# Kernel tuning notes

Hardware: AMD Instinct MI355X
Metric: run time of the kernel (lower is better)

The kernel has to match this reference:

```python
import jax, jax.numpy as jnp
import numpy as np

B, BUFF, STK, NCOMP, HIST = 128, 64, 48, 8, 96
VOCAB, WDIM, POSN, POSD = 100000, 300, 50, 50
DEP, CAD, HAD, FC, U = 40, 50, 50, 128, 256
NOUT = 2 + 2 * DEP


def setup_inputs() -> dict:
    key = jax.random.key(0)
    ks = jax.random.split(key, 40)
    d = {}
    d['buff_word_id'] = jax.random.randint(ks[0], (B, BUFF), 0, VOCAB)
    d['buff_pos_id'] = jax.random.randint(ks[1], (B, BUFF), 0, POSN)
    d['comp_word_id'] = jax.random.randint(ks[2], (B, STK, 2 * NCOMP), 0, VOCAB)
    d['comp_pos_id'] = jax.random.randint(ks[3], (B, STK, 2 * NCOMP), 0, POSN)
    d['comp_action_id'] = jax.random.randint(ks[4], (B, STK, NCOMP), 0, 2 * DEP)
    d['comp_action_len'] = jax.random.randint(ks[5], (B, STK), 0, NCOMP + 1)
    d['history_action_id'] = jax.random.randint(ks[6], (B, HIST), 0, 3 + 4 * DEP)
    d['stack_length'] = jax.random.randint(ks[7], (B,), 1, STK + 1)
    d['buff_length'] = jax.random.randint(ks[8], (B,), 1, BUFF + 1)
    d['history_action_length'] = jax.random.randint(ks[9], (B,), 1, HIST + 1)

    def w(k, shape):
        return jax.random.normal(k, shape, jnp.float32) / np.sqrt(shape[0])

    d['p_emb'] = jax.random.normal(ks[10], (POSN, POSD), jnp.float32) * 0.1
    d['comp_a_emb'] = jax.random.normal(ks[11], (2 * DEP, CAD), jnp.float32) * 0.1
    d['hist_a_emb'] = jax.random.normal(ks[12], (3 + 4 * DEP, HAD), jnp.float32) * 0.1
    d['w_emb'] = jax.random.normal(ks[13], (VOCAB, WDIM), jnp.float32) * 0.1
    d['emb_W'] = w(ks[14], (WDIM + POSD, FC)); d['emb_b'] = jnp.zeros((FC,), jnp.float32)
    d['rec_W'] = w(ks[15], (FC + CAD + FC, FC)); d['rec_b'] = jnp.zeros((FC,), jnp.float32)
    d['sW0'] = w(ks[16], (FC + U, 4 * U)); d['sb0'] = jnp.zeros((4 * U,), jnp.float32)
    d['sW1'] = w(ks[17], (U + U, 4 * U)); d['sb1'] = jnp.zeros((4 * U,), jnp.float32)
    d['bW0'] = w(ks[18], (FC + U, 4 * U)); d['bb0'] = jnp.zeros((4 * U,), jnp.float32)
    d['bW1'] = w(ks[19], (U + U, 4 * U)); d['bb1'] = jnp.zeros((4 * U,), jnp.float32)
    d['aW0'] = w(ks[20], (HAD + U, 4 * U)); d['ab0'] = jnp.zeros((4 * U,), jnp.float32)
    d['aW1'] = w(ks[21], (U + U, 4 * U)); d['ab1'] = jnp.zeros((4 * U,), jnp.float32)
    d['fW'] = w(ks[22], (3 * U, NOUT)); d['fb'] = jnp.zeros((NOUT,), jnp.float32)
    return d


def _lstm_cell(c, h, x, W, b):
    # TF LSTMCell gate order: i, j (candidate), f, o; forget_bias = 1.0
    z = jnp.concatenate([x, h], -1) @ W + b
    i, j, f, o = jnp.split(z, 4, -1)
    c = c * jax.nn.sigmoid(f + 1.0) + jax.nn.sigmoid(i) * jnp.tanh(j)
    h = jnp.tanh(c) * jax.nn.sigmoid(o)
    return c, h


def _run_lstm2(x, lengths, W0, b0, W1, b1):
    # x: [B, T, D]; returns final (at t = length) second-layer h, like dynamic_rnn's state[1].h
    Bb, T, _ = x.shape
    u = W0.shape[1] // 4
    init = tuple(jnp.zeros((Bb, u), x.dtype) for _ in range(4))

    def step(carry, inp):
        xt, t = inp
        c0, h0, c1, h1 = carry
        nc0, nh0 = _lstm_cell(c0, h0, xt, W0, b0)
        nc1, nh1 = _lstm_cell(c1, h1, nh0, W1, b1)
        m = (t < lengths)[:, None]
        new = tuple(jnp.where(m, n, o) for n, o in zip((nc0, nh0, nc1, nh1), carry))
        return new, None

    (c0, h0, c1, h1), _ = jax.lax.scan(step, init, (x.transpose(1, 0, 2), jnp.arange(T)))
    return h1


def _compose(word_id, comp_emb, act_emb, a_len, rec_W, rec_b):
    # word_id: [2N] int, comp_emb: [2N, FC], act_emb: [N, CAD], a_len: scalar
    # Sequential dict-keyed recursive composition (dict keys are head word ids).
    N = act_emb.shape[0]
    head_ids = word_id[0::2]
    dep_ids = word_id[1::2]
    idxs = jnp.arange(N)

    def step(vals, n):
        mask_h = (head_ids == head_ids[n]) & (idxs < n)
        mask_d = (head_ids == dep_ids[n]) & (idxs < n)
        ih = jnp.max(jnp.where(mask_h, idxs, -1))
        idd = jnp.max(jnp.where(mask_d, idxs, -1))
        head_e = jnp.where(ih >= 0, vals[jnp.maximum(ih, 0)], comp_emb[2 * n])
        dep_e = jnp.where(idd >= 0, vals[jnp.maximum(idd, 0)], comp_emb[2 * n + 1])
        new = jnp.tanh(jnp.concatenate([head_e, act_emb[n], dep_e]) @ rec_W + rec_b)
        return vals.at[n].set(new), new

    vals0 = jnp.zeros((N, rec_W.shape[1]), comp_emb.dtype)
    _, news = jax.lax.scan(step, vals0, idxs)
    return jnp.where(a_len == 0, comp_emb[0], news[jnp.maximum(a_len - 1, 0)])


def reference(buff_word_id, buff_pos_id, comp_word_id, comp_pos_id, comp_action_id,
              comp_action_len, history_action_id, stack_length, buff_length,
              history_action_length, p_emb, comp_a_emb, hist_a_emb, w_emb,
              emb_W, emb_b, rec_W, rec_b, sW0, sb0, sW1, sb1, bW0, bb0, bW1, bb1,
              aW0, ab0, aW1, ab1, fW, fb):
    buff_emb = jax.nn.relu(
        jnp.concatenate([w_emb[buff_word_id], p_emb[buff_pos_id]], -1) @ emb_W + emb_b)
    comp_emb = jax.nn.relu(
        jnp.concatenate([w_emb[comp_word_id], p_emb[comp_pos_id]], -1) @ emb_W + emb_b)
    act_emb = comp_a_emb[comp_action_id]        # [B, STK, N, CAD]
    hist_emb = hist_a_emb[history_action_id]    # [B, HIST, HAD]

    comp_fn = lambda wi, ce, ae, al: _compose(wi, ce, ae, al, rec_W, rec_b)
    stack_emb = jax.vmap(jax.vmap(comp_fn))(comp_word_id, comp_emb, act_emb, comp_action_len)

    h_s = _run_lstm2(stack_emb, stack_length, sW0, sb0, sW1, sb1)
    h_b = _run_lstm2(buff_emb, buff_length, bW0, bb0, bW1, bb1)
    h_a = _run_lstm2(hist_emb, history_action_length, aW0, ab0, aW1, ab1)
    return jnp.concatenate([h_s, h_b, h_a], -1) @ fW + fb
```

## Files before the change

kernel.cpp:

```cpp
#include <hip/hip_runtime.h>

#define BB    128
#define BUFF  64
#define STK   48
#define NCOMP 8
#define HIST  96
#define WDIM  300
#define POSD  50
#define CAD   50
#define HAD   50
#define FC    128
#define UU    256
#define NOUT  82

typedef __bf16 bf16;
typedef __attribute__((ext_vector_type(8))) __bf16 bf16x8;
typedef __attribute__((ext_vector_type(4))) float   f32x4;

__device__ __forceinline__ float sigf(float x)   { return 1.f / (1.f + __expf(-x)); }
__device__ __forceinline__ float tanhf_(float x) { return 1.f - 2.f / (1.f + __expf(2.f * x)); }

__device__ __forceinline__ unsigned pack2(const float* p) {
  union { unsigned u; bf16 h[2]; } r;
  r.h[0] = (bf16)p[0]; r.h[1] = (bf16)p[1];
  return r.u;
}

__global__ __launch_bounds__(256) void k_emb(
    const int* bw, const int* bp, const int* cw, const int* cp,
    const float* w_emb, const float* p_emb, const float* embW, const float* embB,
    bf16* comp_emb, bf16* buff_emb)
{
  __shared__ __align__(16) char sm[138752];
  bf16*  A  = (bf16*)sm;
  bf16*  Wt = (bf16*)(sm + 46080);
  float* sb = (float*)(sm + 46080 + 92160);

  const int tid = threadIdx.x;
  const int r0  = blockIdx.x * 64;

  for (int i = tid; i < 64 * 176; i += 256) {
    int m = i / 176, c2 = i % 176, e0 = 2 * c2;
    int r = r0 + m;
    unsigned v;
    if (e0 < 300) {
      int word = (r < 98304) ? cw[r] : bw[r - 98304];
      v = pack2(w_emb + word * 300 + e0);
    } else if (e0 < 350) {
      int pos = (r < 98304) ? cp[r] : bp[r - 98304];
      v = pack2(p_emb + pos * 50 + (e0 - 300));
    } else v = 0u;
    *(unsigned*)(A + m * 360 + e0) = v;
  }
  for (int i = tid; i < 350 * 128; i += 256) {
    int k = i >> 7, n = i & 127;
    Wt[n * 360 + k] = (bf16)embW[i];
  }
  { int i = tid; if (i < 256) { int n = i >> 1; Wt[n * 360 + 350 + (i & 1)] = (bf16)0.f; } }
  if (tid < 128) sb[tid] = embB[tid];
  __syncthreads();

  const int wv = tid >> 6, lane = tid & 63, l15 = lane & 15, quad = lane >> 4;
  f32x4 acc[8];
#pragma unroll
  for (int i = 0; i < 8; ++i) acc[i] = (f32x4){0.f, 0.f, 0.f, 0.f};

  const bf16* Arow = A + (wv * 16 + l15) * 360;
  for (int ks = 0; ks < 11; ++ks) {
    int kq = ks * 32 + quad * 8;
    bf16x8 a = *(const bf16x8*)(Arow + kq);
#pragma unroll
    for (int nt = 0; nt < 8; ++nt) {
      bf16x8 b = *(const bf16x8*)(Wt + (nt * 16 + l15) * 360 + kq);
      acc[nt] = __builtin_amdgcn_mfma_f32_16x16x32_bf16(a, b, acc[nt], 0, 0, 0);
    }
  }
#pragma unroll
  for (int nt = 0; nt < 8; ++nt)
#pragma unroll
    for (int rr = 0; rr < 4; ++rr) {
      int row = wv * 16 + quad * 4 + rr;
      int n   = nt * 16 + l15;
      float z = fmaxf(acc[nt][rr] + sb[n], 0.f);
      int r = r0 + row;
      bf16 o = (bf16)z;
      if (r < 98304) comp_emb[r * 128 + n] = o;
      else           buff_emb[(r - 98304) * 128 + n] = o;
    }
}

__global__ __launch_bounds__(256) void k_compose(
    const int* cw, const int* caid, const int* calen,
    const bf16* comp_emb, const float* ca_emb, const float* recW, const float* recB,
    bf16* stack_emb)
{
  __shared__ __align__(16) char sm[129344];
  bf16*  Wt   = (bf16*)sm;
  bf16*  X    = (bf16*)(sm + 83968);
  bf16*  VALS = (bf16*)(sm + 94464);
  float* recb = (float*)(sm + 127232);
  int*   IH   = (int*)(sm + 127744);
  int*   ID   = (int*)(sm + 128256);
  int*   AN   = (int*)(sm + 128768);
  int*   ALEN = (int*)(sm + 129280);

  const int tid = threadIdx.x;
  const int bs0 = blockIdx.x * 16;

  for (int i = tid; i < 306 * 128; i += 256) {
    int k = i >> 7, n = i & 127;
    Wt[n * 328 + k] = (bf16)recW[i];
  }
  for (int i = tid; i < 128 * 22; i += 256) {
    int n = i / 22, k = 306 + i % 22;
    Wt[n * 328 + k] = (bf16)0.f;
  }
  if (tid < 128) recb[tid] = recB[tid];
  if (tid < 16) {
    int bs = bs0 + tid;
    int hid[8], did[8];
#pragma unroll
    for (int m = 0; m < 8; ++m) { hid[m] = cw[bs * 16 + 2 * m]; did[m] = cw[bs * 16 + 2 * m + 1]; }
    for (int n = 0; n < 8; ++n) {
      int ih = -1, idd = -1;
      for (int m = 0; m < n; ++m) { if (hid[m] == hid[n]) ih = m; if (hid[m] == did[n]) idd = m; }
      IH[tid * 8 + n] = ih; ID[tid * 8 + n] = idd; AN[tid * 8 + n] = caid[bs * 8 + n];
    }
    ALEN[tid] = calen[bs];
  }
  __syncthreads();

  const int wv = tid >> 6, lane = tid & 63, l15 = lane & 15, quad = lane >> 4;

  for (int n = 0; n < 8; ++n) {
    for (int i = tid; i < 16 * 160; i += 256) {
      int p = i / 160, c2 = i % 160, e0 = 2 * c2;
      int bs = bs0 + p;
      unsigned v;
      if (e0 < 128) {
        int ih = IH[p * 8 + n];
        v = (ih >= 0) ? *(const unsigned*)(VALS + (p * 8 + ih) * 128 + e0)
                      : *(const unsigned*)(comp_emb + (bs * 16 + 2 * n) * 128 + e0);
      } else if (e0 < 178) {
        v = pack2(ca_emb + AN[p * 8 + n] * 50 + (e0 - 128));
      } else if (e0 < 306) {
        int e = e0 - 178;
        int idd = ID[p * 8 + n];
        v = (idd >= 0) ? *(const unsigned*)(VALS + (p * 8 + idd) * 128 + e)
                       : *(const unsigned*)(comp_emb + (bs * 16 + 2 * n + 1) * 128 + e);
      } else v = 0u;
      *(unsigned*)(X + p * 328 + e0) = v;
    }
    __syncthreads();

    f32x4 acc[2];
    acc[0] = (f32x4){0.f,0.f,0.f,0.f}; acc[1] = (f32x4){0.f,0.f,0.f,0.f};
    for (int ks = 0; ks < 10; ++ks) {
      int kq = ks * 32 + quad * 8;
      bf16x8 a = *(const bf16x8*)(X + l15 * 328 + kq);
#pragma unroll
      for (int t2 = 0; t2 < 2; ++t2) {
        int nt = 2 * wv + t2;
        bf16x8 b = *(const bf16x8*)(Wt + (nt * 16 + l15) * 328 + kq);
        acc[t2] = __builtin_amdgcn_mfma_f32_16x16x32_bf16(a, b, acc[t2], 0, 0, 0);
      }
    }
    __syncthreads();
#pragma unroll
    for (int t2 = 0; t2 < 2; ++t2) {
      int nt = 2 * wv + t2;
#pragma unroll
      for (int rr = 0; rr < 4; ++rr) {
        int p = quad * 4 + rr;
        int col = nt * 16 + l15;
        VALS[(p * 8 + n) * 128 + col] = (bf16)tanhf_(acc[t2][rr] + recb[col]);
      }
    }
    __syncthreads();
  }

  for (int i = tid; i < 16 * 64; i += 256) {
    int p = i / 64, c2 = i % 64, e0 = 2 * c2;
    int bs = bs0 + p;
    int al = ALEN[p];
    unsigned v = (al == 0) ? *(const unsigned*)(comp_emb + (bs * 16) * 128 + e0)
                           : *(const unsigned*)(VALS + (p * 8 + (al - 1)) * 128 + e0);
    *(unsigned*)(stack_emb + bs * 128 + e0) = v;
  }
}

struct BarT { int cnt; int pad[31]; };

template<int L, int LAYER>
__device__ __forceinline__ void lstm_role(
    const float* W, const float* bias,
    const bf16* xsrc, const float* hist_tab, const int* hist_id,
    const int* lenp, bf16* h0w, bf16* h1w, BarT* bar, char* sm, int u0)
{
  constexpr int T   = (L == 0) ? STK : (L == 1) ? BUFF : HIST;
  constexpr int K   = (LAYER == 0) ? ((L == 2) ? 320 : 384) : 512;
  constexpr int KP  = K + 8;
  constexpr int Kxp = (LAYER == 0) ? ((L == 2) ? 64 : 128) : 256;
  constexpr int Tx  = (L == 0) ? STK : BUFF;

  const int tid = threadIdx.x;
  bf16*  Wt     = (bf16*)sm;
  bf16*  hstage = (bf16*)(sm + 128 * KP * 2);
  float* sb     = (float*)(sm + 128 * KP * 2 + 9216);
  bf16*  Xa     = (bf16*)(sm + 128 * KP * 2 + 9216 + 512);

  for (int i = tid; i < K * 128; i += 256) {
    int kk = i >> 7, cc = i & 127;
    int col = (cc >> 5) * 256 + u0 + (cc & 31);
    bf16 v;
    if (LAYER == 0 && L == 2) {
      if (kk < 64) v = (kk < 50) ? (bf16)W[kk * 1024 + col] : (bf16)0.f;
      else         v = (bf16)W[(kk - 14) * 1024 + col];
    } else v = (bf16)W[kk * 1024 + col];
    Wt[cc * KP + kk] = v;
  }
  if (tid < 128) { int col = (tid >> 5) * 256 + u0 + (tid & 31); sb[tid] = bias[col]; }

  const int wv = tid >> 6, lane = tid & 63, l15 = lane & 15, quad = lane >> 4;
  int lenr[8];
#pragma unroll
  for (int mt = 0; mt < 2; ++mt)
#pragma unroll
    for (int rr = 0; rr < 4; ++rr)
      lenr[mt * 4 + rr] = lenp[32 * wv + 16 * mt + quad * 4 + rr];

  float cst[16], hst[16];
#pragma unroll
  for (int i = 0; i < 16; ++i) { cst[i] = 0.f; hst[i] = 0.f; }

  const int row0 = 32 * wv + l15;

  __syncthreads();

  for (int p = 0; p <= T; ++p) {
    const bool active = (LAYER == 0) ? (p < T) : (p >= 1);
    const int  t = (LAYER == 0) ? p : (p - 1);

    if (L == 2 && LAYER == 0 && active) {
      for (int i = tid; i < 128 * 32; i += 256) {
        int row = i >> 5, e0 = 2 * (i & 31);
        unsigned v = 0u;
        if (e0 < 50) { int id = hist_id[row * 96 + t]; v = pack2(hist_tab + id * 50 + e0); }
        *(unsigned*)(Xa + row * 72 + e0) = v;
      }
    }
    __syncthreads();

    if (active) {
      const bf16* h0r = h0w + ((p - 1) & 1) * 32768;
      const bf16* h1r = h1w + (p & 1) * 32768;

      bf16x8 hA[16];
#pragma unroll
      for (int hk = 0; hk < 8; ++hk)
#pragma unroll
        for (int mt = 0; mt < 2; ++mt) {
          const bf16* pa = h0r + (row0 + 16 * mt) * 256 + hk * 32 + quad * 8;
          asm volatile("global_load_dwordx4 %0, %1, off sc0 sc1"
                       : "=v"(hA[hk * 2 + mt]) : "v"(pa) : "memory");
        }
      bf16x8 hB[16];
      if (LAYER == 1) {
#pragma unroll
        for (int hk = 0; hk < 8; ++hk)
#pragma unroll
          for (int mt = 0; mt < 2; ++mt) {
            const bf16* pb = h1r + (row0 + 16 * mt) * 256 + hk * 32 + quad * 8;
            asm volatile("global_load_dwordx4 %0, %1, off sc0 sc1"
                         : "=v"(hB[hk * 2 + mt]) : "v"(pb) : "memory");
          }
      }

      f32x4 acc[2][8];
#pragma unroll
      for (int a1 = 0; a1 < 2; ++a1)
#pragma unroll
        for (int a2 = 0; a2 < 8; ++a2) acc[a1][a2] = (f32x4){0.f, 0.f, 0.f, 0.f};

      if (LAYER == 0) {
#pragma unroll
        for (int ks = 0; ks < Kxp / 32; ++ks) {
          int kq = ks * 32 + quad * 8;
          bf16x8 a[2];
#pragma unroll
          for (int mt = 0; mt < 2; ++mt) {
            int row = row0 + 16 * mt;
            if (L == 2) a[mt] = *(const bf16x8*)(Xa + row * 72 + kq);
            else        a[mt] = *(const bf16x8*)(xsrc + (row * Tx + t) * 128 + kq);
          }
#pragma unroll
          for (int nt = 0; nt < 8; ++nt) {
            bf16x8 b = *(const bf16x8*)(Wt + (nt * 16 + l15) * KP + kq);
            acc[0][nt] = __builtin_amdgcn_mfma_f32_16x16x32_bf16(a[0], b, acc[0][nt], 0, 0, 0);
            acc[1][nt] = __builtin_amdgcn_mfma_f32_16x16x32_bf16(a[1], b, acc[1][nt], 0, 0, 0);
          }
        }
      }

      asm volatile("s_waitcnt vmcnt(0)" ::: "memory");
      __builtin_amdgcn_sched_barrier(0);

      constexpr int HB0 = (LAYER == 0) ? Kxp : 0;
#pragma unroll
      for (int hk = 0; hk < 8; ++hk) {
        int kq = HB0 + hk * 32 + quad * 8;
#pragma unroll
        for (int nt = 0; nt < 8; ++nt) {
          bf16x8 b = *(const bf16x8*)(Wt + (nt * 16 + l15) * KP + kq);
          acc[0][nt] = __builtin_amdgcn_mfma_f32_16x16x32_bf16(hA[hk * 2 + 0], b, acc[0][nt], 0, 0, 0);
          acc[1][nt] = __builtin_amdgcn_mfma_f32_16x16x32_bf16(hA[hk * 2 + 1], b, acc[1][nt], 0, 0, 0);
        }
      }
      if (LAYER == 1) {
#pragma unroll
        for (int hk = 0; hk < 8; ++hk) {
          int kq = 256 + hk * 32 + quad * 8;
#pragma unroll
          for (int nt = 0; nt < 8; ++nt) {
            bf16x8 b = *(const bf16x8*)(Wt + (nt * 16 + l15) * KP + kq);
            acc[0][nt] = __builtin_amdgcn_mfma_f32_16x16x32_bf16(hB[hk * 2 + 0], b, acc[0][nt], 0, 0, 0);
            acc[1][nt] = __builtin_amdgcn_mfma_f32_16x16x32_bf16(hB[hk * 2 + 1], b, acc[1][nt], 0, 0, 0);
          }
        }
      }

#pragma unroll
      for (int mt = 0; mt < 2; ++mt)
#pragma unroll
        for (int g2 = 0; g2 < 2; ++g2)
#pragma unroll
          for (int rr = 0; rr < 4; ++rr) {
            int row = 32 * wv + 16 * mt + quad * 4 + rr;
            float zi = acc[mt][0 + g2][rr] + sb[(0 + g2) * 16 + l15];
            float zj = acc[mt][2 + g2][rr] + sb[(2 + g2) * 16 + l15];
            float zf = acc[mt][4 + g2][rr] + sb[(4 + g2) * 16 + l15];
            float zo = acc[mt][6 + g2][rr] + sb[(6 + g2) * 16 + l15];
            float ig = sigf(zi), jg = tanhf_(zj), fg = sigf(zf + 1.f), og = sigf(zo);
            int idx = mt * 8 + g2 * 4 + rr;
            float cn = cst[idx] * fg + ig * jg;
            float hn = tanhf_(cn) * og;
            bool mk = (t < lenr[mt * 4 + rr]);
            cst[idx] = mk ? cn : cst[idx];
            hst[idx] = mk ? hn : hst[idx];
            hstage[row * 36 + g2 * 16 + l15] = (bf16)hst[idx];
          }
    }
    __syncthreads();
    if (active) {
      bf16* dst = (LAYER == 0) ? (h0w + (p & 1) * 32768) : (h1w + ((p - 1) & 1) * 32768);
      for (int i = tid; i < 128 * 8; i += 256) {
        int row = i >> 3, c = i & 7;
        unsigned long long v = *(const unsigned long long*)(hstage + row * 36 + c * 4);
        __hip_atomic_store((unsigned long long*)(dst + row * 256 + u0 + c * 4), v,
                           __ATOMIC_RELAXED, __HIP_MEMORY_SCOPE_AGENT);
      }
    }
    if (p < T) {
      __syncthreads();
      if (tid == 0) {
        __builtin_amdgcn_sched_barrier(0);
        const int target = 16 * (p + 1);
        int prev = __hip_atomic_fetch_add(&bar->cnt, 1, __ATOMIC_RELAXED, __HIP_MEMORY_SCOPE_AGENT);
        if (prev != target - 1) {
          while (__hip_atomic_load(&bar->cnt, __ATOMIC_RELAXED, __HIP_MEMORY_SCOPE_AGENT) < target) { }
        }
        __builtin_amdgcn_sched_barrier(0);
      }
      __syncthreads();
    }
  }
}

__global__ __launch_bounds__(256, 1) void k_lstm(
    const float* sW0, const float* sb0, const float* sW1, const float* sb1,
    const float* bW0, const float* bb0, const float* bW1, const float* bb1,
    const float* aW0, const float* ab0, const float* aW1, const float* ab1,
    const bf16* stack_emb, const bf16* buff_emb, const float* hist_tab, const int* hist_id,
    const int* len_s, const int* len_b, const int* len_a,
    bf16* h0buf, bf16* h1buf, BarT* bars)
{
  __shared__ __align__(16) char sm[143872];
  const int bx    = blockIdx.x;
  const int L     = bx >> 4;
  const int rid   = bx & 15;
  const int layer = rid >> 3;
  const int u0    = (rid & 7) * 32;

  BarT* bar = bars + L;
  bf16* h0w = h0buf + L * 2 * 32768;
  bf16* h1w = h1buf + L * 2 * 32768;

  if (L == 0) {
    if (layer == 0) lstm_role<0, 0>(sW0, sb0, stack_emb, hist_tab, hist_id, len_s, h0w, h1w, bar, sm, u0);
    else            lstm_role<0, 1>(sW1, sb1, stack_emb, hist_tab, hist_id, len_s, h0w, h1w, bar, sm, u0);
  } else if (L == 1) {
    if (layer == 0) lstm_role<1, 0>(bW0, bb0, buff_emb, hist_tab, hist_id, len_b, h0w, h1w, bar, sm, u0);
    else            lstm_role<1, 1>(bW1, bb1, buff_emb, hist_tab, hist_id, len_b, h0w, h1w, bar, sm, u0);
  } else {
    if (layer == 0) lstm_role<2, 0>(aW0, ab0, nullptr, hist_tab, hist_id, len_a, h0w, h1w, bar, sm, u0);
    else            lstm_role<2, 1>(aW1, ab1, nullptr, hist_tab, hist_id, len_a, h0w, h1w, bar, sm, u0);
  }
}

__global__ __launch_bounds__(128) void k_final(
    const bf16* h1buf, const float* fW, const float* fb, float* out)
{
  __shared__ float hs[768];
  const int b = blockIdx.x, tid = threadIdx.x;
  for (int i = tid; i < 768; i += 128) {
    int L = i >> 8, u = i & 255;
    hs[i] = (float)h1buf[(L * 2 + 1) * 32768 + b * 256 + u];
  }
  __syncthreads();
  if (tid < NOUT) {
    float acc = fb[tid];
    for (int u = 0; u < 768; ++u) acc += hs[u] * fW[u * NOUT + tid];
    out[b * NOUT + tid] = acc;
  }
}

extern "C" void kernel_launch(void* const* d_in, const int* in_sizes, int n_in,
                              void* d_out, int out_size, void* d_ws, size_t ws_size,
                              hipStream_t stream)
{
  (void)in_sizes; (void)n_in; (void)out_size; (void)ws_size;
  char* ws = (char*)d_ws;
  BarT* bars      = (BarT*)ws;
  bf16* h0buf     = (bf16*)(ws + 512);
  bf16* h1buf     = (bf16*)(ws + 512 + 393216);
  bf16* comp_emb  = (bf16*)(ws + 786944);
  bf16* buff_emb  = (bf16*)(ws + 786944 + 25165824);
  bf16* stack_emb = (bf16*)(ws + 786944 + 25165824 + 2097152);

  hipMemsetAsync(ws, 0, 786944, stream);

  k_emb<<<1664, 256, 0, stream>>>(
      (const int*)d_in[0], (const int*)d_in[1], (const int*)d_in[2], (const int*)d_in[3],
      (const float*)d_in[13], (const float*)d_in[10], (const float*)d_in[14], (const float*)d_in[15],
      comp_emb, buff_emb);

  k_compose<<<384, 256, 0, stream>>>(
      (const int*)d_in[2], (const int*)d_in[4], (const int*)d_in[5],
      comp_emb, (const float*)d_in[11], (const float*)d_in[16], (const float*)d_in[17],
      stack_emb);

  k_lstm<<<48, 256, 0, stream>>>(
      (const float*)d_in[18], (const float*)d_in[19], (const float*)d_in[20], (const float*)d_in[21],
      (const float*)d_in[22], (const float*)d_in[23], (const float*)d_in[24], (const float*)d_in[25],
      (const float*)d_in[26], (const float*)d_in[27], (const float*)d_in[28], (const float*)d_in[29],
      stack_emb, buff_emb, (const float*)d_in[12], (const int*)d_in[6],
      (const int*)d_in[7], (const int*)d_in[8], (const int*)d_in[9],
      h0buf, h1buf, bars);

  k_final<<<128, 128, 0, stream>>>(h1buf, (const float*)d_in[30], (const float*)d_in[31],
                                   (float*)d_out);
}
```

Before: 1.944 ms.

## Place each LSTM group on one XCD and relax coherence for intra-XCD exchange

The LSTM kernel now launches 256 blocks. Each block reads its XCC id from a hardware register and claims a role slot so that all 16 blocks of one LSTM sit on the same XCD; blocks that find no slot exit. Once a group is placed, it checks that every member shares the XCC id and that probe stores are visible. If both hold, the hidden-state exchange uses L2-coherent loads (sc0 only) and plain stores instead of system-scope loads and atomic stores, which aims to cut the latency of the cross-block recurrent exchange. The cost is extra startup work: the claim, a wait of up to about 10k ticks for blocks that must fall back, and a slot-claim barrier. It also relies on undocumented placement and coherence behaviour.

```diff
diff --git a/kernel.cpp b/kernel.cpp
--- a/kernel.cpp
+++ b/kernel.cpp
@@ -191,7 +191,25 @@
 
 struct BarT { int cnt; int pad[31]; };
 
-template<int L, int LAYER>
+template<bool COH>
+__device__ __forceinline__ bf16x8 hload(const bf16* p) {
+  bf16x8 v;
+  if constexpr (COH)
+    asm volatile("global_load_dwordx4 %0, %1, off sc0" : "=v"(v) : "v"(p) : "memory");
+  else
+    asm volatile("global_load_dwordx4 %0, %1, off sc0 sc1" : "=v"(v) : "v"(p) : "memory");
+  return v;
+}
+
+template<bool COH>
+__device__ __forceinline__ void hstore(bf16* p, unsigned long long v) {
+  if constexpr (COH)
+    asm volatile("global_store_dwordx2 %0, %1, off" :: "v"(p), "v"(v) : "memory");
+  else
+    __hip_atomic_store((unsigned long long*)p, v, __ATOMIC_RELAXED, __HIP_MEMORY_SCOPE_AGENT);
+}
+
+template<int L, int LAYER, bool COH>
 __device__ __forceinline__ void lstm_role(
     const float* W, const float* bias,
     const bf16* xsrc, const float* hist_tab, const int* hist_id,
@@ -259,21 +277,15 @@
 #pragma unroll
       for (int hk = 0; hk < 8; ++hk)
 #pragma unroll
-        for (int mt = 0; mt < 2; ++mt) {
-          const bf16* pa = h0r + (row0 + 16 * mt) * 256 + hk * 32 + quad * 8;
-          asm volatile("global_load_dwordx4 %0, %1, off sc0 sc1"
-                       : "=v"(hA[hk * 2 + mt]) : "v"(pa) : "memory");
-        }
+        for (int mt = 0; mt < 2; ++mt)
+          hA[hk * 2 + mt] = hload<COH>(h0r + (row0 + 16 * mt) * 256 + hk * 32 + quad * 8);
       bf16x8 hB[16];
       if (LAYER == 1) {
 #pragma unroll
         for (int hk = 0; hk < 8; ++hk)
 #pragma unroll
-          for (int mt = 0; mt < 2; ++mt) {
-            const bf16* pb = h1r + (row0 + 16 * mt) * 256 + hk * 32 + quad * 8;
-            asm volatile("global_load_dwordx4 %0, %1, off sc0 sc1"
-                         : "=v"(hB[hk * 2 + mt]) : "v"(pb) : "memory");
-          }
+          for (int mt = 0; mt < 2; ++mt)
+            hB[hk * 2 + mt] = hload<COH>(h1r + (row0 + 16 * mt) * 256 + hk * 32 + quad * 8);
       }
 
       f32x4 acc[2][8];
@@ -356,8 +368,7 @@
       for (int i = tid; i < 128 * 8; i += 256) {
         int row = i >> 3, c = i & 7;
         unsigned long long v = *(const unsigned long long*)(hstage + row * 36 + c * 4);
-        __hip_atomic_store((unsigned long long*)(dst + row * 256 + u0 + c * 4), v,
-                           __ATOMIC_RELAXED, __HIP_MEMORY_SCOPE_AGENT);
+        hstore<COH>(dst + row * 256 + u0 + c * 4, v);
       }
     }
     if (p < T) {
@@ -382,28 +393,88 @@
     const float* aW0, const float* ab0, const float* aW1, const float* ab1,
     const bf16* stack_emb, const bf16* buff_emb, const float* hist_tab, const int* hist_id,
     const int* len_s, const int* len_b, const int* len_a,
-    bf16* h0buf, bf16* h1buf, BarT* bars)
+    bf16* h0buf, bf16* h1buf, BarT* bars, BarT* cbars, int* taken, int* xcctab, int* probes)
 {
   __shared__ __align__(16) char sm[143872];
-  const int bx    = blockIdx.x;
-  const int L     = bx >> 4;
-  const int rid   = bx & 15;
+  __shared__ int s_role[3];
+  const int tid = threadIdx.x;
+
+  if (tid == 0) {
+    int xcc = __builtin_amdgcn_s_getreg(6164) & 0xF;
+    int l = -1, r = -1;
+    if (xcc < 3) {
+      int st = blockIdx.x & 15;
+      for (int ii = 0; ii < 16 && l < 0; ++ii) {
+        int i = (st + ii) & 15;
+        int exp0 = 0;
+        if (__hip_atomic_compare_exchange_strong(&taken[xcc * 16 + i], &exp0, 1,
+              __ATOMIC_RELAXED, __ATOMIC_RELAXED, __HIP_MEMORY_SCOPE_AGENT)) { l = xcc; r = i; }
+      }
+    }
+    if (l < 0) {
+      unsigned long long t0 = __builtin_amdgcn_s_memrealtime();
+      while (__builtin_amdgcn_s_memrealtime() - t0 < 10000ULL) __builtin_amdgcn_s_sleep(16);
+      for (int i = 0; i < 48 && l < 0; ++i) {
+        int exp0 = 0;
+        if (__hip_atomic_compare_exchange_strong(&taken[i], &exp0, 1,
+              __ATOMIC_RELAXED, __ATOMIC_RELAXED, __HIP_MEMORY_SCOPE_AGENT)) { l = i >> 4; r = i & 15; }
+      }
+    }
+    s_role[0] = l; s_role[1] = r; s_role[2] = 0;
+    if (l >= 0) {
+      __hip_atomic_store(&xcctab[l * 16 + r], xcc + 1, __ATOMIC_RELAXED, __HIP_MEMORY_SCOPE_AGENT);
+      int* pp = &probes[l * 16 + r];
+      int tok = r + 1;
+      asm volatile("global_store_dword %0, %1, off" :: "v"(pp), "v"(tok) : "memory");
+      asm volatile("s_waitcnt vmcnt(0)" ::: "memory");
+      __hip_atomic_fetch_add(&cbars[l].cnt, 1, __ATOMIC_RELAXED, __HIP_MEMORY_SCOPE_AGENT);
+      while (__hip_atomic_load(&cbars[l].cnt, __ATOMIC_RELAXED, __HIP_MEMORY_SCOPE_AGENT) < 16)
+        __builtin_amdgcn_s_sleep(1);
+      int myx = xcc + 1, coh = 1;
+      for (int i = 0; i < 16; ++i)
+        coh &= (__hip_atomic_load(&xcctab[l * 16 + i], __ATOMIC_RELAXED, __HIP_MEMORY_SCOPE_AGENT) == myx);
+      for (int i = 0; i < 16; ++i) {
+        int* qp = &probes[l * 16 + i];
+        int pv;
+        asm volatile("global_load_dword %0, %1, off sc0" : "=v"(pv) : "v"(qp) : "memory");
+        asm volatile("s_waitcnt vmcnt(0)" ::: "memory");
+        coh &= (pv == i + 1);
+      }
+      s_role[2] = coh;
+    }
+  }
+  __syncthreads();
+
+  const int l = s_role[0];
+  if (l < 0) return;
+  const int rid = s_role[1], coh = s_role[2];
   const int layer = rid >> 3;
   const int u0    = (rid & 7) * 32;
 
-  BarT* bar = bars + L;
-  bf16* h0w = h0buf + L * 2 * 32768;
-  bf16* h1w = h1buf + L * 2 * 32768;
-
-  if (L == 0) {
-    if (layer == 0) lstm_role<0, 0>(sW0, sb0, stack_emb, hist_tab, hist_id, len_s, h0w, h1w, bar, sm, u0);
-    else            lstm_role<0, 1>(sW1, sb1, stack_emb, hist_tab, hist_id, len_s, h0w, h1w, bar, sm, u0);
-  } else if (L == 1) {
-    if (layer == 0) lstm_role<1, 0>(bW0, bb0, buff_emb, hist_tab, hist_id, len_b, h0w, h1w, bar, sm, u0);
-    else            lstm_role<1, 1>(bW1, bb1, buff_emb, hist_tab, hist_id, len_b, h0w, h1w, bar, sm, u0);
-  } else {
-    if (layer == 0) lstm_role<2, 0>(aW0, ab0, nullptr, hist_tab, hist_id, len_a, h0w, h1w, bar, sm, u0);
-    else            lstm_role<2, 1>(aW1, ab1, nullptr, hist_tab, hist_id, len_a, h0w, h1w, bar, sm, u0);
+  BarT* bar = bars + l;
+  bf16* h0w = h0buf + l * 2 * 32768;
+  bf16* h1w = h1buf + l * 2 * 32768;
+
+  const float *W0_, *b0_, *W1_, *b1_; const bf16* xs_; const int* lenp_;
+  if (l == 0)      { W0_ = sW0; b0_ = sb0; W1_ = sW1; b1_ = sb1; xs_ = stack_emb; lenp_ = len_s; }
+  else if (l == 1) { W0_ = bW0; b0_ = bb0; W1_ = bW1; b1_ = bb1; xs_ = buff_emb;  lenp_ = len_b; }
+  else             { W0_ = aW0; b0_ = ab0; W1_ = aW1; b1_ = ab1; xs_ = nullptr;   lenp_ = len_a; }
+  const float* W  = layer ? W1_ : W0_;
+  const float* bi = layer ? b1_ : b0_;
+
+  switch (l * 4 + layer * 2 + coh) {
+    case  0: lstm_role<0, 0, false>(W, bi, xs_, hist_tab, hist_id, lenp_, h0w, h1w, bar, sm, u0); break;
+    case  1: lstm_role<0, 0, true >(W, bi, xs_, hist_tab, hist_id, lenp_, h0w, h1w, bar, sm, u0); break;
+    case  2: lstm_role<0, 1, false>(W, bi, xs_, hist_tab, hist_id, lenp_, h0w, h1w, bar, sm, u0); break;
+    case  3: lstm_role<0, 1, true >(W, bi, xs_, hist_tab, hist_id, lenp_, h0w, h1w, bar, sm, u0); break;
+    case  4: lstm_role<1, 0, false>(W, bi, xs_, hist_tab, hist_id, lenp_, h0w, h1w, bar, sm, u0); break;
+    case  5: lstm_role<1, 0, true >(W, bi, xs_, hist_tab, hist_id, lenp_, h0w, h1w, bar, sm, u0); break;
+    case  6: lstm_role<1, 1, false>(W, bi, xs_, hist_tab, hist_id, lenp_, h0w, h1w, bar, sm, u0); break;
+    case  7: lstm_role<1, 1, true >(W, bi, xs_, hist_tab, hist_id, lenp_, h0w, h1w, bar, sm, u0); break;
+    case  8: lstm_role<2, 0, false>(W, bi, xs_, hist_tab, hist_id, lenp_, h0w, h1w, bar, sm, u0); break;
+    case  9: lstm_role<2, 0, true >(W, bi, xs_, hist_tab, hist_id, lenp_, h0w, h1w, bar, sm, u0); break;
+    case 10: lstm_role<2, 1, false>(W, bi, xs_, hist_tab, hist_id, lenp_, h0w, h1w, bar, sm, u0); break;
+    case 11: lstm_role<2, 1, true >(W, bi, xs_, hist_tab, hist_id, lenp_, h0w, h1w, bar, sm, u0); break;
   }
 }
 
@@ -430,14 +501,18 @@
 {
   (void)in_sizes; (void)n_in; (void)out_size; (void)ws_size;
   char* ws = (char*)d_ws;
-  BarT* bars      = (BarT*)ws;
-  bf16* h0buf     = (bf16*)(ws + 512);
-  bf16* h1buf     = (bf16*)(ws + 512 + 393216);
-  bf16* comp_emb  = (bf16*)(ws + 786944);
-  bf16* buff_emb  = (bf16*)(ws + 786944 + 25165824);
-  bf16* stack_emb = (bf16*)(ws + 786944 + 25165824 + 2097152);
-
-  hipMemsetAsync(ws, 0, 786944, stream);
+  BarT* bars   = (BarT*)ws;
+  BarT* cbars  = (BarT*)(ws + 512);
+  int*  taken  = (int*)(ws + 1024);
+  int*  xcctab = (int*)(ws + 1280);
+  int*  probes = (int*)(ws + 1536);
+  bf16* h0buf  = (bf16*)(ws + 2048);
+  bf16* h1buf  = (bf16*)(ws + 2048 + 393216);
+  bf16* comp_emb  = (bf16*)(ws + 788480);
+  bf16* buff_emb  = (bf16*)(ws + 788480 + 25165824);
+  bf16* stack_emb = (bf16*)(ws + 788480 + 25165824 + 2097152);
+
+  hipMemsetAsync(ws, 0, 788480, stream);
 
   k_emb<<<1664, 256, 0, stream>>>(
       (const int*)d_in[0], (const int*)d_in[1], (const int*)d_in[2], (const int*)d_in[3],
@@ -449,13 +524,13 @@
       comp_emb, (const float*)d_in[11], (const float*)d_in[16], (const float*)d_in[17],
       stack_emb);
 
-  k_lstm<<<48, 256, 0, stream>>>(
+  k_lstm<<<256, 256, 0, stream>>>(
       (const float*)d_in[18], (const float*)d_in[19], (const float*)d_in[20], (const float*)d_in[21],
       (const float*)d_in[22], (const float*)d_in[23], (const float*)d_in[24], (const float*)d_in[25],
       (const float*)d_in[26], (const float*)d_in[27], (const float*)d_in[28], (const float*)d_in[29],
       stack_emb, buff_emb, (const float*)d_in[12], (const int*)d_in[6],
       (const int*)d_in[7], (const int*)d_in[8], (const int*)d_in[9],
-      h0buf, h1buf, bars);
+      h0buf, h1buf, bars, cbars, taken, xcctab, probes);
 
   k_final<<<128, 128, 0, stream>>>(h1buf, (const float*)d_in[30], (const float*)d_in[31],
                                    (float*)d_out);
```

Result: faster. 1.888 ms (-2.9%).
